# Kernel tuning notes

Measured on AMD Instinct MI355X. Metric: run time of the kernel, lower is better.

The kernel has to match this reference:

```python
import jax, jax.numpy as jnp
import numpy as np

S = 64            # rendered_size
CLASS_NUM = 14    # dataset.enc_len
NEG_SLOPE = 0.01
EPS = 1e-5


def _conv(x, w, stride, pad):
    return jax.lax.conv_general_dilated(
        x, w, (stride, stride), [(pad, pad), (pad, pad)],
        dimension_numbers=("NCHW", "OIHW", "NCHW"))


def _bn(x, gamma, beta):
    # BatchNorm2d in training mode: biased batch stats over (N,H,W)
    m = jnp.mean(x, axis=(0, 2, 3), keepdims=True)
    v = jnp.var(x, axis=(0, 2, 3), keepdims=True)
    xn = (x - m) * jax.lax.rsqrt(v + EPS)
    return xn * gamma.reshape(1, -1, 1, 1) + beta.reshape(1, -1, 1, 1)


def _lrelu(x):
    return jnp.where(x >= 0, x, NEG_SLOPE * x)


def _render(elements):
    # elements: (B, N, class_num+4)
    rects = elements[:, :, -4:]
    cls = elements[:, :, :-4]                       # (B, N, C)
    x = rects[:, :, 0][:, :, None, None] * S        # (B, N, 1, 1)
    y = rects[:, :, 1][:, :, None, None] * S
    w = rects[:, :, 2][:, :, None, None] * S
    h = rects[:, :, 3][:, :, None, None] * S
    x0, x1 = x - 0.5 * w, x + 0.5 * w
    y0, y1 = y - 0.5 * h, y + 0.5 * h
    cx = jnp.arange(S, dtype=elements.dtype)[None, None, None, :]  # varies along W
    cy = jnp.arange(S, dtype=elements.dtype)[None, None, :, None]  # varies along H
    k = lambda c, cr: jnp.maximum(1.0 - jnp.abs(c - cr), 0.0)
    b0 = lambda c, cr: jnp.clip(c - cr, 0.0, 1.0)
    b1 = lambda cr, c: jnp.clip(cr - c, 0.0, 1.0)
    by = b0(cy, y0) * b1(y1, cy)                    # (B, N, S, S)
    bx = b0(cx, x0) * b1(x1, cx)
    l0 = k(cx, x0) * by
    l1 = k(cx, x1) * by
    l2 = k(cy, y0) * bx
    l3 = k(cy, y1) * bx
    rendered = jnp.maximum(jnp.maximum(l0, l1), jnp.maximum(l2, l3))  # (B,N,S,S)
    # sum over elements of class one-hot * rendered -> (B, C, S, S)
    return jnp.einsum("bnc,bnhw->bchw", cls, rendered)


def setup_inputs() -> dict:
    key = jax.random.key(0)
    ks = jax.random.split(key, 8)
    B, N = 64, 46
    inp = {
        "input_data": jax.random.uniform(ks[0], (B, N, CLASS_NUM + 4), dtype=jnp.float32),
        "input_length": jax.random.randint(ks[1], (B,), 0, N, dtype=jnp.int32),
        # cnn convs (bias=False) + BN affine params
        "w1": jax.random.normal(ks[2], (64, CLASS_NUM, 5, 5), jnp.float32) * 0.05,
        "g1": jnp.ones((64,), jnp.float32), "b1": jnp.zeros((64,), jnp.float32),
        "w2": jax.random.normal(ks[3], (128, 64, 5, 5), jnp.float32) * 0.03,
        "g2": jnp.ones((128,), jnp.float32), "b2": jnp.zeros((128,), jnp.float32),
        "w3": jax.random.normal(ks[4], (256, 128, 5, 5), jnp.float32) * 0.02,
        "g3": jnp.ones((256,), jnp.float32), "b3": jnp.zeros((256,), jnp.float32),
        # classifier: conv k=8 (bias=False) + BN + 1x1 conv (bias=True)
        "w4": jax.random.normal(ks[5], (1024, 256, 8, 8), jnp.float32) * 0.01,
        "g4": jnp.ones((1024,), jnp.float32), "b4": jnp.zeros((1024,), jnp.float32),
        "w5": jax.random.normal(ks[6], (1, 1024, 1, 1), jnp.float32) * 0.03,
        "b5": jnp.zeros((1,), jnp.float32),
    }
    return inp


def reference(input_data, input_length, w1, g1, b1, w2, g2, b2,
              w3, g3, b3, w4, g4, b4, w5, b5):
    rendered = _render(input_data)                       # (B, C, 64, 64)
    h = _lrelu(_bn(_conv(rendered, w1, 2, 2), g1, b1))   # (B, 64, 32, 32)
    h = _lrelu(_bn(_conv(h, w2, 2, 2), g2, b2))          # (B, 128, 16, 16)
    h = _lrelu(_bn(_conv(h, w3, 2, 2), g3, b3))          # (B, 256, 8, 8)
    h = _lrelu(_bn(_conv(h, w4, 1, 0), g4, b4))          # (B, 1024, 1, 1)
    out = _conv(h, w5, 1, 0) + b5.reshape(1, -1, 1, 1)   # (B, 1, 1, 1)
    return out.squeeze()                                 # (B,)
```

## Files before the change

### kernel.cpp

```cpp
#include <hip/hip_runtime.h>
#include <hip/hip_bf16.h>

#define NEG 0.01f
#define EPS 1e-5f

typedef __attribute__((ext_vector_type(8))) short short8;
typedef __attribute__((ext_vector_type(4))) float floatx4;

__device__ inline unsigned short f2bf(float f) {
    __hip_bfloat16 h = __float2bfloat16(f);
    union { __hip_bfloat16 h; unsigned short u; } cv; cv.h = h;
    return cv.u;
}

__global__ __launch_bounds__(256) void render_kernel(const float* __restrict__ in,
                                                     unsigned short* __restrict__ out) {
    int b = blockIdx.x >> 4;
    int chunk = blockIdx.x & 15;
    __shared__ float r0[46], r1[46], r2[46], r3[46];
    __shared__ float cls_s[46 * 14];
    int tid = threadIdx.x;
    if (tid < 46) {
        const float* p = in + ((size_t)b * 46 + tid) * 18 + 14;
        float x = p[0] * 64.f, y = p[1] * 64.f, w = p[2] * 64.f, h = p[3] * 64.f;
        r0[tid] = x - 0.5f * w; r1[tid] = x + 0.5f * w;
        r2[tid] = y - 0.5f * h; r3[tid] = y + 0.5f * h;
    }
    for (int idx = tid; idx < 46 * 14; idx += 256) {
        int n = idx / 14, c = idx % 14;
        cls_s[idx] = in[((size_t)b * 46 + n) * 18 + c];
    }
    __syncthreads();
    if (tid < 33) {
        int j = chunk * 33 + tid;
        if (j < 528) {
            int y, x;
            if (j < 136) { y = j / 68; x = j - y * 68; }
            else if (j < 272) { int t = j - 136; int yy = t / 68; y = 66 + yy; x = t - yy * 68; }
            else { int t = j - 272; y = 2 + (t >> 2); int k = t & 3; x = (k < 2) ? k : 64 + k; }
            size_t zb = (((size_t)b * 68 + y) * 68 + x) * 16;
            short8 z;
#pragma unroll
            for (int i = 0; i < 8; ++i) z[i] = 0;
            *(short8*)(out + zb) = z;
            *(short8*)(out + zb + 8) = z;
        }
    }
    int pix = chunk * 256 + tid;
    float cx = (float)(pix & 63);
    float cy = (float)(pix >> 6);
    float acc[14];
#pragma unroll
    for (int c = 0; c < 14; ++c) acc[c] = 0.f;
    for (int n = 0; n < 46; ++n) {
        float x0 = r0[n], x1 = r1[n], y0 = r2[n], y1 = r3[n];
        float by = fminf(fmaxf(cy - y0, 0.f), 1.f) * fminf(fmaxf(y1 - cy, 0.f), 1.f);
        float bx = fminf(fmaxf(cx - x0, 0.f), 1.f) * fminf(fmaxf(x1 - cx, 0.f), 1.f);
        float kx0 = fmaxf(1.f - fabsf(cx - x0), 0.f);
        float kx1 = fmaxf(1.f - fabsf(cx - x1), 0.f);
        float ky0 = fmaxf(1.f - fabsf(cy - y0), 0.f);
        float ky1 = fmaxf(1.f - fabsf(cy - y1), 0.f);
        float r = fmaxf(fmaxf(kx0 * by, kx1 * by), fmaxf(ky0 * bx, ky1 * bx));
        if (r > 0.f) {
#pragma unroll
            for (int c = 0; c < 14; ++c) acc[c] = fmaf(cls_s[n * 14 + c], r, acc[c]);
        }
    }
    size_t obase = (((size_t)b * 68 + ((pix >> 6) + 2)) * 68 + ((pix & 63) + 2)) * 16;
    short8 v0, v1;
#pragma unroll
    for (int i = 0; i < 8; ++i) v0[i] = (short)f2bf(acc[i]);
#pragma unroll
    for (int i = 0; i < 6; ++i) v1[i] = (short)f2bf(acc[8 + i]);
    v1[6] = 0; v1[7] = 0;
    *(short8*)(out + obase) = v0;
    *(short8*)(out + obase + 8) = v1;
}

__global__ __launch_bounds__(256) void wtrans_all(const float* __restrict__ w1,
                                                  const float* __restrict__ w2,
                                                  const float* __restrict__ w3,
                                                  unsigned short* __restrict__ wT1,
                                                  unsigned short* __restrict__ wT2,
                                                  unsigned short* __restrict__ wT3) {
    int idx = blockIdx.x * 256 + threadIdx.x;
    const float* w; unsigned short* wT; int CIN, CPLOG, SUB, COLOG;
    if (idx < 30720) { w = w1; wT = wT1; CIN = 14; CPLOG = 4; SUB = 3; COLOG = 6; }
    else if (idx < 235520) { idx -= 30720; w = w2; wT = wT2; CIN = 64; CPLOG = 6; SUB = 10; COLOG = 7; }
    else if (idx < 1054720) { idx -= 235520; w = w3; wT = wT3; CIN = 128; CPLOG = 7; SUB = 20; COLOG = 8; }
    else return;
    int kk = idx & 31;
    int co = (idx >> 5) & ((1 << COLOG) - 1);
    int s = idx >> (5 + COLOG);
    int kh = s / SUB, sub = s - kh * SUB;
    int kidx = sub * 32 + kk;
    int kw = kidx >> CPLOG;
    int ci = kidx & ((1 << CPLOG) - 1);
    float v = (kw < 5 && ci < CIN) ? w[((size_t)(co * CIN + ci) * 5 + kh) * 5 + kw] : 0.f;
    wT[idx] = f2bf(v);
}

template <int CP, int COUT, int HP, int LOG_OHW, int LOG_OW, int SUB,
          int NCO, int NT, int CH, int NW>
__global__ __launch_bounds__(NW * 64) void conv_mfma(
        const unsigned short* __restrict__ inP,
        const unsigned short* __restrict__ wT,
        float* __restrict__ outX,
        float* __restrict__ stacc) {
    constexpr int NSTEP = 5 * SUB;
    constexpr int NCHUNK = NSTEP / CH;
    constexpr int COT = NT * 16;
    constexpr int NSTG = (CH * COT * 4) / (NW * 64);
    static_assert(NSTEP % CH == 0, "CH must divide NSTEP");
    static_assert((CH * COT * 4) % (NW * 64) == 0, "staging must tile evenly");
    __shared__ short Bs[2][CH][COT][32];
    __shared__ float sred[NW][2][COT];
    int tid = threadIdx.x;
    int wave = tid >> 6, lane = tid & 63, q = lane >> 4, l16 = lane & 15;
    int bm = blockIdx.x / NCO, bco = blockIdx.x % NCO;

    const short* aB[4];
#pragma unroll
    for (int f = 0; f < 4; ++f) {
        int m = bm * (NW * 64) + wave * 64 + f * 16 + l16;
        int b = m >> LOG_OHW;
        int ohw = m & ((1 << LOG_OHW) - 1);
        int oh = ohw >> LOG_OW, ow = ohw & ((1 << LOG_OW) - 1);
        aB[f] = (const short*)inP + ((size_t)((b * HP + 2 * oh) * HP + 2 * ow)) * CP + q * 8;
    }
    const short* bgbase = (const short*)wT + (size_t)bco * COT * 32;

    floatx4 acc[4][NT];
#pragma unroll
    for (int f = 0; f < 4; ++f)
#pragma unroll
        for (int nt = 0; nt < NT; ++nt) acc[f][nt] = (floatx4){0.f, 0.f, 0.f, 0.f};

    short8 nb[NSTG];
#pragma unroll
    for (int i = 0; i < NSTG; ++i) {
        int v = tid + i * NW * 64;
        int s = v / (COT * 4);
        int rem = v - s * (COT * 4);
        nb[i] = *(const short8*)(bgbase + ((size_t)s * COUT) * 32 + rem * 8);
    }
#pragma unroll
    for (int i = 0; i < NSTG; ++i) {
        int v = tid + i * NW * 64;
        int s = v / (COT * 4);
        int rem = v - s * (COT * 4);
        *(short8*)((short*)&Bs[0][s][0][0] + rem * 8) = nb[i];
    }
    __syncthreads();

    for (int chunk = 0; chunk < NCHUNK; ++chunk) {
        int cur = chunk & 1;
        if (chunk + 1 < NCHUNK) {
            int step0 = (chunk + 1) * CH;
#pragma unroll
            for (int i = 0; i < NSTG; ++i) {
                int v = tid + i * NW * 64;
                int s = v / (COT * 4);
                int rem = v - s * (COT * 4);
                nb[i] = *(const short8*)(bgbase + ((size_t)(step0 + s) * COUT) * 32 + rem * 8);
            }
        }
#pragma unroll
        for (int s = 0; s < CH; ++s) {
            int step = chunk * CH + s;
            int kh = step / SUB, sub = step - kh * SUB;
            short8 af[4];
#pragma unroll
            for (int f = 0; f < 4; ++f)
                af[f] = *(const short8*)(aB[f] + (size_t)(kh * HP) * CP + sub * 32);
#pragma unroll
            for (int nt = 0; nt < NT; ++nt) {
                short8 bf = *(const short8*)&Bs[cur][s][nt * 16 + l16][q * 8];
#pragma unroll
                for (int f = 0; f < 4; ++f)
                    acc[f][nt] = __builtin_amdgcn_mfma_f32_16x16x32_bf16(af[f], bf, acc[f][nt], 0, 0, 0);
            }
        }
        if (chunk + 1 < NCHUNK) {
#pragma unroll
            for (int i = 0; i < NSTG; ++i) {
                int v = tid + i * NW * 64;
                int s = v / (COT * 4);
                int rem = v - s * (COT * 4);
                *(short8*)((short*)&Bs[cur ^ 1][s][0][0] + rem * 8) = nb[i];
            }
            __syncthreads();
        }
    }
#pragma unroll
    for (int f = 0; f < 4; ++f)
#pragma unroll
        for (int nt = 0; nt < NT; ++nt)
#pragma unroll
            for (int rg = 0; rg < 4; ++rg) {
                int mg = bm * (NW * 64) + wave * 64 + f * 16 + q * 4 + rg;
                int co = bco * COT + nt * 16 + l16;
                outX[(size_t)mg * COUT + co] = acc[f][nt][rg];
            }
#pragma unroll
    for (int nt = 0; nt < NT; ++nt) {
        float s = 0.f, s2 = 0.f;
#pragma unroll
        for (int f = 0; f < 4; ++f)
#pragma unroll
            for (int rg = 0; rg < 4; ++rg) {
                float v = acc[f][nt][rg];
                s += v; s2 = fmaf(v, v, s2);
            }
        s += __shfl_xor(s, 16); s += __shfl_xor(s, 32);
        s2 += __shfl_xor(s2, 16); s2 += __shfl_xor(s2, 32);
        if (q == 0) {
            sred[wave][0][nt * 16 + l16] = s;
            sred[wave][1][nt * 16 + l16] = s2;
        }
    }
    __syncthreads();
    if (tid < COT) {
        float ts = 0.f, ts2 = 0.f;
#pragma unroll
        for (int w = 0; w < NW; ++w) { ts += sred[w][0][tid]; ts2 += sred[w][1][tid]; }
        atomicAdd(&stacc[bco * COT + tid], ts);
        atomicAdd(&stacc[COUT + bco * COT + tid], ts2);
    }
}

__global__ __launch_bounds__(256) void conv4_mfma(const unsigned short* __restrict__ A,
                                                  const float* __restrict__ w4,
                                                  float* __restrict__ h4) {
    constexpr int CH = 4, NCHUNK = 8;
    __shared__ short Bs[CH][64][40];
    int tid = threadIdx.x;
    int bco = blockIdx.x & 15;
    int ks = blockIdx.x >> 4;
    int wave = tid >> 6, lane = tid & 63, q = lane >> 4, l16 = lane & 15;
    const short* aBase = (const short*)A + (size_t)(wave * 16 + l16) * 16384 + ks * 1024 + q * 8;
    int r = tid >> 2, cc = tid & 3;
    const float* bg = w4 + (size_t)(bco * 64 + r) * 16384 + ks * 1024 + cc * 8;

    floatx4 acc[4];
#pragma unroll
    for (int nt = 0; nt < 4; ++nt) acc[nt] = (floatx4){0.f, 0.f, 0.f, 0.f};

    short8 nb[CH];
#pragma unroll
    for (int s = 0; s < CH; ++s) {
        float4 b0 = *(const float4*)(bg + s * 32);
        float4 b1 = *(const float4*)(bg + s * 32 + 4);
        nb[s][0] = (short)f2bf(b0.x); nb[s][1] = (short)f2bf(b0.y);
        nb[s][2] = (short)f2bf(b0.z); nb[s][3] = (short)f2bf(b0.w);
        nb[s][4] = (short)f2bf(b1.x); nb[s][5] = (short)f2bf(b1.y);
        nb[s][6] = (short)f2bf(b1.z); nb[s][7] = (short)f2bf(b1.w);
    }
#pragma unroll
    for (int s = 0; s < CH; ++s) *(short8*)&Bs[s][r][cc * 8] = nb[s];
    __syncthreads();

    for (int chunk = 0; chunk < NCHUNK; ++chunk) {
        bool has_next = (chunk + 1 < NCHUNK);
        if (has_next) {
#pragma unroll
            for (int s = 0; s < CH; ++s) {
                int step = (chunk + 1) * CH + s;
                float4 b0 = *(const float4*)(bg + step * 32);
                float4 b1 = *(const float4*)(bg + step * 32 + 4);
                nb[s][0] = (short)f2bf(b0.x); nb[s][1] = (short)f2bf(b0.y);
                nb[s][2] = (short)f2bf(b0.z); nb[s][3] = (short)f2bf(b0.w);
                nb[s][4] = (short)f2bf(b1.x); nb[s][5] = (short)f2bf(b1.y);
                nb[s][6] = (short)f2bf(b1.z); nb[s][7] = (short)f2bf(b1.w);
            }
        }
#pragma unroll
        for (int s = 0; s < CH; ++s) {
            int step = chunk * CH + s;
            short8 af = *(const short8*)(aBase + step * 32);
#pragma unroll
            for (int nt = 0; nt < 4; ++nt) {
                short8 bf = *(const short8*)&Bs[s][nt * 16 + l16][q * 8];
                acc[nt] = __builtin_amdgcn_mfma_f32_16x16x32_bf16(af, bf, acc[nt], 0, 0, 0);
            }
        }
        if (has_next) {
            __syncthreads();
#pragma unroll
            for (int s = 0; s < CH; ++s) *(short8*)&Bs[s][r][cc * 8] = nb[s];
            __syncthreads();
        }
    }
#pragma unroll
    for (int nt = 0; nt < 4; ++nt) {
#pragma unroll
        for (int rg = 0; rg < 4; ++rg) {
            int mg = wave * 16 + q * 4 + rg;
            int co = bco * 64 + nt * 16 + l16;
            atomicAdd(&h4[(size_t)mg * 1024 + co], acc[nt][rg]);
        }
    }
}

__global__ __launch_bounds__(256) void stats_part(const float* __restrict__ X,
                                                  float* __restrict__ acc,
                                                  int CO, int R, int RPB, int CGLOG) {
    int tid = threadIdx.x;
    int cg = blockIdx.x & ((1 << CGLOG) - 1);
    int rb = blockIdx.x >> CGLOG;
    int c = (cg << 6) + (tid & 63);
    int w = tid >> 6;
    float s = 0.f, s2 = 0.f;
    int rend = min(R, (rb + 1) * RPB);
    for (int r = rb * RPB + w; r < rend; r += 4) {
        float v = X[(size_t)r * CO + c];
        s += v; s2 += v * v;
    }
    __shared__ float ls[4][64], ls2[4][64];
    ls[w][tid & 63] = s; ls2[w][tid & 63] = s2;
    __syncthreads();
    if (tid < 64) {
        float ts = ls[0][tid] + ls[1][tid] + ls[2][tid] + ls[3][tid];
        float ts2 = ls2[0][tid] + ls2[1][tid] + ls2[2][tid] + ls2[3][tid];
        int cc = (cg << 6) + tid;
        atomicAdd(&acc[cc], ts);
        atomicAdd(&acc[CO + cc], ts2);
    }
}

__global__ __launch_bounds__(256) void bnpad_kernel(const float* __restrict__ X,
                                                    const float* __restrict__ stacc,
                                                    const float* __restrict__ g,
                                                    const float* __restrict__ bb,
                                                    unsigned short* __restrict__ out,
                                                    int CO_LOG, int OH, int OHP,
                                                    float invN, int total) {
    int idx = blockIdx.x * 256 + threadIdx.x;
    if (idx >= total) return;
    int CO = 1 << CO_LOG;
    int c = idx & (CO - 1);
    float mean = stacc[c] * invN;
    float var = fmaxf(stacc[CO + c] * invN - mean * mean, 0.f);
    float sc = g[c] * rsqrtf(var + EPS);
    float sh = bb[c] - mean * sc;
    int t = idx >> CO_LOG;
    int x = t % OHP; t /= OHP;
    int y = t % OHP; int b = t / OHP;
    unsigned short v = 0;
    if (y >= 2 && y < OH + 2 && x >= 2 && x < OH + 2) {
        float f = X[(((size_t)(b * OH + (y - 2)) * OH + (x - 2)) << CO_LOG) + c];
        f = f * sc + sh;
        f = f >= 0.f ? f : NEG * f;
        v = f2bf(f);
    }
    out[idx] = v;
}

__global__ __launch_bounds__(256) void bn_nchw_kernel(const float* __restrict__ X,
                                                      const float* __restrict__ stacc,
                                                      const float* __restrict__ g,
                                                      const float* __restrict__ bb,
                                                      unsigned short* __restrict__ out,
                                                      int total) {
    int idx = blockIdx.x * 256 + threadIdx.x;
    if (idx >= total) return;
    int hw = idx & 63;
    int ci = (idx >> 6) & 255;
    int b = idx >> 14;
    float mean = stacc[ci] * (1.f / 4096.f);
    float var = fmaxf(stacc[256 + ci] * (1.f / 4096.f) - mean * mean, 0.f);
    float sc = g[ci] * rsqrtf(var + EPS);
    float sh = bb[ci] - mean * sc;
    float f = X[((size_t)(b * 64 + hw)) * 256 + ci] * sc + sh;
    f = f >= 0.f ? f : NEG * f;
    out[idx] = f2bf(f);
}

__global__ __launch_bounds__(256) void conv5_kernel(const float* __restrict__ X,
                                                    const float* __restrict__ stacc,
                                                    const float* __restrict__ g,
                                                    const float* __restrict__ bb,
                                                    const float* __restrict__ w5,
                                                    const float* __restrict__ b5,
                                                    float* __restrict__ out) {
    int b = blockIdx.x, tid = threadIdx.x;
    float s = 0.f;
    for (int c = tid; c < 1024; c += 256) {
        float mean = stacc[c] * (1.f / 64.f);
        float var = fmaxf(stacc[1024 + c] * (1.f / 64.f) - mean * mean, 0.f);
        float sc = g[c] * rsqrtf(var + EPS);
        float sh = bb[c] - mean * sc;
        float f = X[(size_t)b * 1024 + c] * sc + sh;
        f = f >= 0.f ? f : NEG * f;
        s = fmaf(f, w5[c], s);
    }
#pragma unroll
    for (int off = 32; off > 0; off >>= 1) s += __shfl_down(s, off);
    __shared__ float ls[4];
    if ((tid & 63) == 0) ls[tid >> 6] = s;
    __syncthreads();
    if (tid == 0) out[b] = ls[0] + ls[1] + ls[2] + ls[3] + b5[0];
}

extern "C" void kernel_launch(void* const* d_in, const int* in_sizes, int n_in,
                              void* d_out, int out_size, void* d_ws, size_t ws_size,
                              hipStream_t stream) {
    (void)in_sizes; (void)n_in; (void)out_size; (void)ws_size;
    const float* input_data = (const float*)d_in[0];
    const float* w1 = (const float*)d_in[2];
    const float* g1 = (const float*)d_in[3];
    const float* b1 = (const float*)d_in[4];
    const float* w2 = (const float*)d_in[5];
    const float* g2 = (const float*)d_in[6];
    const float* b2 = (const float*)d_in[7];
    const float* w3 = (const float*)d_in[8];
    const float* g3 = (const float*)d_in[9];
    const float* b3 = (const float*)d_in[10];
    const float* w4 = (const float*)d_in[11];
    const float* g4 = (const float*)d_in[12];
    const float* b4 = (const float*)d_in[13];
    const float* w5 = (const float*)d_in[14];
    const float* b5 = (const float*)d_in[15];

    char* ws = (char*)d_ws;
    float* regA = (float*)ws;
    char* wsB = ws + 16777216;
    char* wsC = wsB + 10616832;
    char* wsD = wsC + 9469952;
    float* h4  = (float*)wsD;
    float* st1 = (float*)(wsD + 262144);
    float* st2 = (float*)(wsD + 262656);
    float* st3 = (float*)(wsD + 263680);
    float* st4 = (float*)(wsD + 265728);
    unsigned short* wT1 = (unsigned short*)(wsD + 274432);
    unsigned short* wT2 = (unsigned short*)(wsD + 335872);
    unsigned short* wT3 = (unsigned short*)(wsD + 745472);

    unsigned short* rendered = (unsigned short*)wsC;
    float* conv1out = regA;
    unsigned short* pad1 = (unsigned short*)wsB;
    float* conv2out = (float*)wsC;
    unsigned short* pad2 = (unsigned short*)wsB;
    float* conv3out = regA;
    unsigned short* a4 = (unsigned short*)wsC;

    hipMemsetAsync(wsD, 0, 273920, stream);
    wtrans_all<<<4120, 256, 0, stream>>>(w1, w2, w3, wT1, wT2, wT3);
    render_kernel<<<1024, 256, 0, stream>>>(input_data, rendered);

    conv_mfma<16, 64, 68, 10, 5, 3, 1, 4, 5, 4><<<256, 256, 0, stream>>>(rendered, wT1, conv1out, st1);
    bnpad_kernel<<<20736, 256, 0, stream>>>(conv1out, st1, g1, b1, pad1, 6, 32, 36, 1.f / 65536.f, 5308416);

    conv_mfma<64, 128, 36, 8, 4, 10, 4, 2, 10, 4><<<256, 256, 0, stream>>>(pad1, wT2, conv2out, st2);
    bnpad_kernel<<<12800, 256, 0, stream>>>(conv2out, st2, g2, b2, pad2, 7, 16, 20, 1.f / 16384.f, 3276800);

    conv_mfma<128, 256, 20, 6, 3, 20, 8, 2, 10, 2><<<256, 128, 0, stream>>>(pad2, wT3, conv3out, st3);
    bn_nchw_kernel<<<4096, 256, 0, stream>>>(conv3out, st3, g3, b3, a4, 1048576);

    conv4_mfma<<<256, 256, 0, stream>>>(a4, w4, h4);
    stats_part<<<16, 256, 0, stream>>>(h4, st4, 1024, 64, 64, 4);

    conv5_kernel<<<64, 256, 0, stream>>>(h4, st4, g4, b4, w5, b5, (float*)d_out);
}
```

Before: 278.9 us.

## Stream conv weight fragments directly from global memory instead of LDS staging

All conv kernels drop the double-buffered LDS staging of weight tiles and the __syncthreads barriers. Each lane now loads its B fragments straight from global memory every k-step, and the k loop is fully unrolled over kh and sub. Tile shapes change: conv2 and conv3 use fewer waves with wider output-channel tiles per wave, and conv4 becomes a single-wave kernel that computes 4x4 MFMA tiles per lane. This removes barrier and LDS traffic, but weights are re-read from global memory or L2 by more waves, grids keep only 256 blocks of 1 to 4 waves, and register pressure rises.

```diff
diff --git a/kernel.cpp b/kernel.cpp
--- a/kernel.cpp
+++ b/kernel.cpp
@@ -101,19 +101,13 @@
 }
 
 template <int CP, int COUT, int HP, int LOG_OHW, int LOG_OW, int SUB,
-          int NCO, int NT, int CH, int NW>
-__global__ __launch_bounds__(NW * 64) void conv_mfma(
+          int NCO, int NT, int NW>
+__global__ __launch_bounds__(NW * 64) void conv_stream(
         const unsigned short* __restrict__ inP,
         const unsigned short* __restrict__ wT,
         float* __restrict__ outX,
         float* __restrict__ stacc) {
-    constexpr int NSTEP = 5 * SUB;
-    constexpr int NCHUNK = NSTEP / CH;
     constexpr int COT = NT * 16;
-    constexpr int NSTG = (CH * COT * 4) / (NW * 64);
-    static_assert(NSTEP % CH == 0, "CH must divide NSTEP");
-    static_assert((CH * COT * 4) % (NW * 64) == 0, "staging must tile evenly");
-    __shared__ short Bs[2][CH][COT][32];
     __shared__ float sred[NW][2][COT];
     int tid = threadIdx.x;
     int wave = tid >> 6, lane = tid & 63, q = lane >> 4, l16 = lane & 15;
@@ -128,7 +122,7 @@
         int oh = ohw >> LOG_OW, ow = ohw & ((1 << LOG_OW) - 1);
         aB[f] = (const short*)inP + ((size_t)((b * HP + 2 * oh) * HP + 2 * ow)) * CP + q * 8;
     }
-    const short* bgbase = (const short*)wT + (size_t)bco * COT * 32;
+    const short* bB = (const short*)wT + (size_t)(bco * COT + l16) * 32 + q * 8;
 
     floatx4 acc[4][NT];
 #pragma unroll
@@ -136,60 +130,24 @@
 #pragma unroll
         for (int nt = 0; nt < NT; ++nt) acc[f][nt] = (floatx4){0.f, 0.f, 0.f, 0.f};
 
-    short8 nb[NSTG];
-#pragma unroll
-    for (int i = 0; i < NSTG; ++i) {
-        int v = tid + i * NW * 64;
-        int s = v / (COT * 4);
-        int rem = v - s * (COT * 4);
-        nb[i] = *(const short8*)(bgbase + ((size_t)s * COUT) * 32 + rem * 8);
-    }
-#pragma unroll
-    for (int i = 0; i < NSTG; ++i) {
-        int v = tid + i * NW * 64;
-        int s = v / (COT * 4);
-        int rem = v - s * (COT * 4);
-        *(short8*)((short*)&Bs[0][s][0][0] + rem * 8) = nb[i];
-    }
-    __syncthreads();
-
-    for (int chunk = 0; chunk < NCHUNK; ++chunk) {
-        int cur = chunk & 1;
-        if (chunk + 1 < NCHUNK) {
-            int step0 = (chunk + 1) * CH;
-#pragma unroll
-            for (int i = 0; i < NSTG; ++i) {
-                int v = tid + i * NW * 64;
-                int s = v / (COT * 4);
-                int rem = v - s * (COT * 4);
-                nb[i] = *(const short8*)(bgbase + ((size_t)(step0 + s) * COUT) * 32 + rem * 8);
-            }
-        }
-#pragma unroll
-        for (int s = 0; s < CH; ++s) {
-            int step = chunk * CH + s;
-            int kh = step / SUB, sub = step - kh * SUB;
+#pragma unroll
+    for (int kh = 0; kh < 5; ++kh) {
+#pragma unroll
+        for (int sub = 0; sub < SUB; ++sub) {
+            int step = kh * SUB + sub;
             short8 af[4];
 #pragma unroll
             for (int f = 0; f < 4; ++f)
                 af[f] = *(const short8*)(aB[f] + (size_t)(kh * HP) * CP + sub * 32);
-#pragma unroll
-            for (int nt = 0; nt < NT; ++nt) {
-                short8 bf = *(const short8*)&Bs[cur][s][nt * 16 + l16][q * 8];
+            short8 bf[NT];
+#pragma unroll
+            for (int nt = 0; nt < NT; ++nt)
+                bf[nt] = *(const short8*)(bB + (size_t)step * COUT * 32 + nt * 512);
+#pragma unroll
+            for (int nt = 0; nt < NT; ++nt)
 #pragma unroll
                 for (int f = 0; f < 4; ++f)
-                    acc[f][nt] = __builtin_amdgcn_mfma_f32_16x16x32_bf16(af[f], bf, acc[f][nt], 0, 0, 0);
-            }
-        }
-        if (chunk + 1 < NCHUNK) {
-#pragma unroll
-            for (int i = 0; i < NSTG; ++i) {
-                int v = tid + i * NW * 64;
-                int s = v / (COT * 4);
-                int rem = v - s * (COT * 4);
-                *(short8*)((short*)&Bs[cur ^ 1][s][0][0] + rem * 8) = nb[i];
-            }
-            __syncthreads();
+                    acc[f][nt] = __builtin_amdgcn_mfma_f32_16x16x32_bf16(af[f], bf[nt], acc[f][nt], 0, 0, 0);
         }
     }
 #pragma unroll
@@ -202,6 +160,7 @@
                 int co = bco * COT + nt * 16 + l16;
                 outX[(size_t)mg * COUT + co] = acc[f][nt][rg];
             }
+    float ps[NT], ps2[NT];
 #pragma unroll
     for (int nt = 0; nt < NT; ++nt) {
         float s = 0.f, s2 = 0.f;
@@ -214,92 +173,87 @@
             }
         s += __shfl_xor(s, 16); s += __shfl_xor(s, 32);
         s2 += __shfl_xor(s2, 16); s2 += __shfl_xor(s2, 32);
+        ps[nt] = s; ps2[nt] = s2;
+    }
+    if (NW == 1) {
         if (q == 0) {
-            sred[wave][0][nt * 16 + l16] = s;
-            sred[wave][1][nt * 16 + l16] = s2;
-        }
-    }
-    __syncthreads();
-    if (tid < COT) {
-        float ts = 0.f, ts2 = 0.f;
-#pragma unroll
-        for (int w = 0; w < NW; ++w) { ts += sred[w][0][tid]; ts2 += sred[w][1][tid]; }
-        atomicAdd(&stacc[bco * COT + tid], ts);
-        atomicAdd(&stacc[COUT + bco * COT + tid], ts2);
-    }
-}
-
-__global__ __launch_bounds__(256) void conv4_mfma(const unsigned short* __restrict__ A,
-                                                  const float* __restrict__ w4,
-                                                  float* __restrict__ h4) {
-    constexpr int CH = 4, NCHUNK = 8;
-    __shared__ short Bs[CH][64][40];
-    int tid = threadIdx.x;
+#pragma unroll
+            for (int nt = 0; nt < NT; ++nt) {
+                int co = bco * COT + nt * 16 + l16;
+                atomicAdd(&stacc[co], ps[nt]);
+                atomicAdd(&stacc[COUT + co], ps2[nt]);
+            }
+        }
+    } else {
+        if (q == 0) {
+#pragma unroll
+            for (int nt = 0; nt < NT; ++nt) {
+                sred[wave][0][nt * 16 + l16] = ps[nt];
+                sred[wave][1][nt * 16 + l16] = ps2[nt];
+            }
+        }
+        __syncthreads();
+        if (tid < COT) {
+            float ts = 0.f, ts2 = 0.f;
+#pragma unroll
+            for (int w = 0; w < NW; ++w) { ts += sred[w][0][tid]; ts2 += sred[w][1][tid]; }
+            atomicAdd(&stacc[bco * COT + tid], ts);
+            atomicAdd(&stacc[COUT + bco * COT + tid], ts2);
+        }
+    }
+}
+
+__global__ __launch_bounds__(64) void conv4_stream(const unsigned short* __restrict__ A,
+                                                   const float* __restrict__ w4,
+                                                   float* __restrict__ h4) {
+    int lane = threadIdx.x, q = lane >> 4, l16 = lane & 15;
     int bco = blockIdx.x & 15;
     int ks = blockIdx.x >> 4;
-    int wave = tid >> 6, lane = tid & 63, q = lane >> 4, l16 = lane & 15;
-    const short* aBase = (const short*)A + (size_t)(wave * 16 + l16) * 16384 + ks * 1024 + q * 8;
-    int r = tid >> 2, cc = tid & 3;
-    const float* bg = w4 + (size_t)(bco * 64 + r) * 16384 + ks * 1024 + cc * 8;
-
-    floatx4 acc[4];
-#pragma unroll
-    for (int nt = 0; nt < 4; ++nt) acc[nt] = (floatx4){0.f, 0.f, 0.f, 0.f};
-
-    short8 nb[CH];
-#pragma unroll
-    for (int s = 0; s < CH; ++s) {
-        float4 b0 = *(const float4*)(bg + s * 32);
-        float4 b1 = *(const float4*)(bg + s * 32 + 4);
-        nb[s][0] = (short)f2bf(b0.x); nb[s][1] = (short)f2bf(b0.y);
-        nb[s][2] = (short)f2bf(b0.z); nb[s][3] = (short)f2bf(b0.w);
-        nb[s][4] = (short)f2bf(b1.x); nb[s][5] = (short)f2bf(b1.y);
-        nb[s][6] = (short)f2bf(b1.z); nb[s][7] = (short)f2bf(b1.w);
-    }
-#pragma unroll
-    for (int s = 0; s < CH; ++s) *(short8*)&Bs[s][r][cc * 8] = nb[s];
-    __syncthreads();
-
-    for (int chunk = 0; chunk < NCHUNK; ++chunk) {
-        bool has_next = (chunk + 1 < NCHUNK);
-        if (has_next) {
-#pragma unroll
-            for (int s = 0; s < CH; ++s) {
-                int step = (chunk + 1) * CH + s;
-                float4 b0 = *(const float4*)(bg + step * 32);
-                float4 b1 = *(const float4*)(bg + step * 32 + 4);
-                nb[s][0] = (short)f2bf(b0.x); nb[s][1] = (short)f2bf(b0.y);
-                nb[s][2] = (short)f2bf(b0.z); nb[s][3] = (short)f2bf(b0.w);
-                nb[s][4] = (short)f2bf(b1.x); nb[s][5] = (short)f2bf(b1.y);
-                nb[s][6] = (short)f2bf(b1.z); nb[s][7] = (short)f2bf(b1.w);
+    const short* aB[4];
+#pragma unroll
+    for (int f = 0; f < 4; ++f)
+        aB[f] = (const short*)A + (size_t)(f * 16 + l16) * 16384 + ks * 1024 + q * 8;
+    const float* bB = w4 + (size_t)(bco * 64 + l16) * 16384 + ks * 1024 + q * 8;
+
+    floatx4 acc[4][4];
+#pragma unroll
+    for (int f = 0; f < 4; ++f)
+#pragma unroll
+        for (int nt = 0; nt < 4; ++nt) acc[f][nt] = (floatx4){0.f, 0.f, 0.f, 0.f};
+
+#pragma unroll 8
+    for (int step = 0; step < 32; ++step) {
+        short8 af[4];
+#pragma unroll
+        for (int f = 0; f < 4; ++f)
+            af[f] = *(const short8*)(aB[f] + step * 32);
+        short8 bf[4];
+#pragma unroll
+        for (int nt = 0; nt < 4; ++nt) {
+            const float* p = bB + (size_t)nt * 16 * 16384 + step * 32;
+            float4 b0 = *(const float4*)p;
+            float4 b1 = *(const float4*)(p + 4);
+            bf[nt][0] = (short)f2bf(b0.x); bf[nt][1] = (short)f2bf(b0.y);
+            bf[nt][2] = (short)f2bf(b0.z); bf[nt][3] = (short)f2bf(b0.w);
+            bf[nt][4] = (short)f2bf(b1.x); bf[nt][5] = (short)f2bf(b1.y);
+            bf[nt][6] = (short)f2bf(b1.z); bf[nt][7] = (short)f2bf(b1.w);
+        }
+#pragma unroll
+        for (int nt = 0; nt < 4; ++nt)
+#pragma unroll
+            for (int f = 0; f < 4; ++f)
+                acc[f][nt] = __builtin_amdgcn_mfma_f32_16x16x32_bf16(af[f], bf[nt], acc[f][nt], 0, 0, 0);
+    }
+#pragma unroll
+    for (int f = 0; f < 4; ++f)
+#pragma unroll
+        for (int nt = 0; nt < 4; ++nt)
+#pragma unroll
+            for (int rg = 0; rg < 4; ++rg) {
+                int mg = f * 16 + q * 4 + rg;
+                int co = bco * 64 + nt * 16 + l16;
+                atomicAdd(&h4[(size_t)mg * 1024 + co], acc[f][nt][rg]);
             }
-        }
-#pragma unroll
-        for (int s = 0; s < CH; ++s) {
-            int step = chunk * CH + s;
-            short8 af = *(const short8*)(aBase + step * 32);
-#pragma unroll
-            for (int nt = 0; nt < 4; ++nt) {
-                short8 bf = *(const short8*)&Bs[s][nt * 16 + l16][q * 8];
-                acc[nt] = __builtin_amdgcn_mfma_f32_16x16x32_bf16(af, bf, acc[nt], 0, 0, 0);
-            }
-        }
-        if (has_next) {
-            __syncthreads();
-#pragma unroll
-            for (int s = 0; s < CH; ++s) *(short8*)&Bs[s][r][cc * 8] = nb[s];
-            __syncthreads();
-        }
-    }
-#pragma unroll
-    for (int nt = 0; nt < 4; ++nt) {
-#pragma unroll
-        for (int rg = 0; rg < 4; ++rg) {
-            int mg = wave * 16 + q * 4 + rg;
-            int co = bco * 64 + nt * 16 + l16;
-            atomicAdd(&h4[(size_t)mg * 1024 + co], acc[nt][rg]);
-        }
-    }
 }
 
 __global__ __launch_bounds__(256) void stats_part(const float* __restrict__ X,
@@ -448,16 +402,16 @@
     wtrans_all<<<4120, 256, 0, stream>>>(w1, w2, w3, wT1, wT2, wT3);
     render_kernel<<<1024, 256, 0, stream>>>(input_data, rendered);
 
-    conv_mfma<16, 64, 68, 10, 5, 3, 1, 4, 5, 4><<<256, 256, 0, stream>>>(rendered, wT1, conv1out, st1);
+    conv_stream<16, 64, 68, 10, 5, 3, 1, 4, 4><<<256, 256, 0, stream>>>(rendered, wT1, conv1out, st1);
     bnpad_kernel<<<20736, 256, 0, stream>>>(conv1out, st1, g1, b1, pad1, 6, 32, 36, 1.f / 65536.f, 5308416);
 
-    conv_mfma<64, 128, 36, 8, 4, 10, 4, 2, 10, 4><<<256, 256, 0, stream>>>(pad1, wT2, conv2out, st2);
+    conv_stream<64, 128, 36, 8, 4, 10, 2, 4, 2><<<256, 128, 0, stream>>>(pad1, wT2, conv2out, st2);
     bnpad_kernel<<<12800, 256, 0, stream>>>(conv2out, st2, g2, b2, pad2, 7, 16, 20, 1.f / 16384.f, 3276800);
 
-    conv_mfma<128, 256, 20, 6, 3, 20, 8, 2, 10, 2><<<256, 128, 0, stream>>>(pad2, wT3, conv3out, st3);
+    conv_stream<128, 256, 20, 6, 3, 20, 4, 4, 1><<<256, 64, 0, stream>>>(pad2, wT3, conv3out, st3);
     bn_nchw_kernel<<<4096, 256, 0, stream>>>(conv3out, st3, g3, b3, a4, 1048576);
 
-    conv4_mfma<<<256, 256, 0, stream>>>(a4, w4, h4);
+    conv4_stream<<<256, 64, 0, stream>>>(a4, w4, h4);
     stats_part<<<16, 256, 0, stream>>>(h4, st4, 1024, 64, 64, 4);
 
     conv5_kernel<<<64, 256, 0, stream>>>(h4, st4, g4, b4, w5, b5, (float*)d_out);
```

Result: slower. 365.4 us (+31.0%).

## Split-K conv2 and conv3 into partial buffers to raise block parallelism

Applied to the files above, without the earlier changes.

Adds a conv_split kernel that divides the reduction steps of conv2 (2-way) and conv3 (4-way) across extra blocks, launching 1024 blocks of 128 threads instead of 256 blocks. Each split writes its partial outputs to its own buffer. Separate stats_part launches then sum the partials and compute BN statistics, and the BN/pad kernels also sum the partials. This is meant to fill more compute units on the mid-size convolutions, at the cost of extra partial-output traffic, re-reading the partials twice, and two extra kernel launches. The workspace layout is rearranged so the partial buffers do not alias each other.

```diff
diff --git a/kernel.cpp b/kernel.cpp
--- a/kernel.cpp
+++ b/kernel.cpp
@@ -111,8 +111,6 @@
     constexpr int NCHUNK = NSTEP / CH;
     constexpr int COT = NT * 16;
     constexpr int NSTG = (CH * COT * 4) / (NW * 64);
-    static_assert(NSTEP % CH == 0, "CH must divide NSTEP");
-    static_assert((CH * COT * 4) % (NW * 64) == 0, "staging must tile evenly");
     __shared__ short Bs[2][CH][COT][32];
     __shared__ float sred[NW][2][COT];
     int tid = threadIdx.x;
@@ -227,6 +225,114 @@
         atomicAdd(&stacc[bco * COT + tid], ts);
         atomicAdd(&stacc[COUT + bco * COT + tid], ts2);
     }
+}
+
+template <int CP, int COUT, int HP, int LOG_OHW, int LOG_OW, int SUB,
+          int NM, int NCO, int NT, int CH, int NW, int KS>
+__global__ __launch_bounds__(NW * 64) void conv_split(
+        const unsigned short* __restrict__ inP,
+        const unsigned short* __restrict__ wT,
+        float* __restrict__ outP) {
+    constexpr int NSTEP = 5 * SUB;
+    constexpr int SSTEP = NSTEP / KS;
+    constexpr int NCHUNK = SSTEP / CH;
+    constexpr int COT = NT * 16;
+    constexpr int NSTG = (CH * COT * 4) / (NW * 64);
+    constexpr int M = NM * NW * 64;
+    static_assert(NSTEP % KS == 0 && SSTEP % CH == 0, "split tiling");
+    __shared__ short Bs[2][CH][COT][32];
+    int tid = threadIdx.x;
+    int wave = tid >> 6, lane = tid & 63, q = lane >> 4, l16 = lane & 15;
+    int bidx = blockIdx.x;
+    int ks = bidx / (NM * NCO);
+    int rem = bidx - ks * (NM * NCO);
+    int bm = rem / NCO, bco = rem % NCO;
+    int sbase = ks * SSTEP;
+
+    const short* aB[4];
+#pragma unroll
+    for (int f = 0; f < 4; ++f) {
+        int m = bm * (NW * 64) + wave * 64 + f * 16 + l16;
+        int b = m >> LOG_OHW;
+        int ohw = m & ((1 << LOG_OHW) - 1);
+        int oh = ohw >> LOG_OW, ow = ohw & ((1 << LOG_OW) - 1);
+        aB[f] = (const short*)inP + ((size_t)((b * HP + 2 * oh) * HP + 2 * ow)) * CP + q * 8;
+    }
+    const short* bgbase = (const short*)wT + (size_t)bco * COT * 32;
+
+    floatx4 acc[4][NT];
+#pragma unroll
+    for (int f = 0; f < 4; ++f)
+#pragma unroll
+        for (int nt = 0; nt < NT; ++nt) acc[f][nt] = (floatx4){0.f, 0.f, 0.f, 0.f};
+
+    short8 nb[NSTG];
+#pragma unroll
+    for (int i = 0; i < NSTG; ++i) {
+        int v = tid + i * NW * 64;
+        int s = v / (COT * 4);
+        int rem2 = v - s * (COT * 4);
+        nb[i] = *(const short8*)(bgbase + ((size_t)(sbase + s) * COUT) * 32 + rem2 * 8);
+    }
+#pragma unroll
+    for (int i = 0; i < NSTG; ++i) {
+        int v = tid + i * NW * 64;
+        int s = v / (COT * 4);
+        int rem2 = v - s * (COT * 4);
+        *(short8*)((short*)&Bs[0][s][0][0] + rem2 * 8) = nb[i];
+    }
+    __syncthreads();
+
+    for (int chunk = 0; chunk < NCHUNK; ++chunk) {
+        int cur = chunk & 1;
+        if (chunk + 1 < NCHUNK) {
+            int step0 = sbase + (chunk + 1) * CH;
+#pragma unroll
+            for (int i = 0; i < NSTG; ++i) {
+                int v = tid + i * NW * 64;
+                int s = v / (COT * 4);
+                int rem2 = v - s * (COT * 4);
+                nb[i] = *(const short8*)(bgbase + ((size_t)(step0 + s) * COUT) * 32 + rem2 * 8);
+            }
+        }
+#pragma unroll
+        for (int s = 0; s < CH; ++s) {
+            int gstep = sbase + chunk * CH + s;
+            int kh = gstep / SUB, sub = gstep - kh * SUB;
+            short8 af[4];
+#pragma unroll
+            for (int f = 0; f < 4; ++f)
+                af[f] = *(const short8*)(aB[f] + (size_t)(kh * HP) * CP + sub * 32);
+#pragma unroll
+            for (int nt = 0; nt < NT; ++nt) {
+                short8 bf = *(const short8*)&Bs[cur][s][nt * 16 + l16][q * 8];
+#pragma unroll
+                for (int f = 0; f < 4; ++f)
+                    acc[f][nt] = __builtin_amdgcn_mfma_f32_16x16x32_bf16(af[f], bf, acc[f][nt], 0, 0, 0);
+            }
+        }
+        if (chunk + 1 < NCHUNK) {
+#pragma unroll
+            for (int i = 0; i < NSTG; ++i) {
+                int v = tid + i * NW * 64;
+                int s = v / (COT * 4);
+                int rem2 = v - s * (COT * 4);
+                *(short8*)((short*)&Bs[cur ^ 1][s][0][0] + rem2 * 8) = nb[i];
+            }
+            __syncthreads();
+        }
+    }
+    float* outK = outP + (size_t)ks * M * COUT;
+#pragma unroll
+    for (int f = 0; f < 4; ++f)
+#pragma unroll
+        for (int nt = 0; nt < NT; ++nt)
+#pragma unroll
+            for (int rg = 0; rg < 4; ++rg) {
+                int mg = bm * (NW * 64) + wave * 64 + f * 16 + q * 4 + rg;
+                int co = bco * COT + nt * 16 + l16;
+                outK[(size_t)mg * COUT + co] = acc[f][nt][rg];
+            }
 }
 
 __global__ __launch_bounds__(256) void conv4_mfma(const unsigned short* __restrict__ A,
@@ -304,7 +410,8 @@
 
 __global__ __launch_bounds__(256) void stats_part(const float* __restrict__ X,
                                                   float* __restrict__ acc,
-                                                  int CO, int R, int RPB, int CGLOG) {
+                                                  int CO, int R, int RPB, int CGLOG,
+                                                  int nsplit, size_t kstride) {
     int tid = threadIdx.x;
     int cg = blockIdx.x & ((1 << CGLOG) - 1);
     int rb = blockIdx.x >> CGLOG;
@@ -313,7 +420,8 @@
     float s = 0.f, s2 = 0.f;
     int rend = min(R, (rb + 1) * RPB);
     for (int r = rb * RPB + w; r < rend; r += 4) {
-        float v = X[(size_t)r * CO + c];
+        float v = 0.f;
+        for (int t = 0; t < nsplit; ++t) v += X[(size_t)t * kstride + (size_t)r * CO + c];
         s += v; s2 += v * v;
     }
     __shared__ float ls[4][64], ls2[4][64];
@@ -334,7 +442,8 @@
                                                     const float* __restrict__ bb,
                                                     unsigned short* __restrict__ out,
                                                     int CO_LOG, int OH, int OHP,
-                                                    float invN, int total) {
+                                                    float invN, int total,
+                                                    int nsplit, size_t kstride) {
     int idx = blockIdx.x * 256 + threadIdx.x;
     if (idx >= total) return;
     int CO = 1 << CO_LOG;
@@ -348,7 +457,9 @@
     int y = t % OHP; int b = t / OHP;
     unsigned short v = 0;
     if (y >= 2 && y < OH + 2 && x >= 2 && x < OH + 2) {
-        float f = X[(((size_t)(b * OH + (y - 2)) * OH + (x - 2)) << CO_LOG) + c];
+        size_t base = (((size_t)(b * OH + (y - 2)) * OH + (x - 2)) << CO_LOG) + c;
+        float f = 0.f;
+        for (int ts = 0; ts < nsplit; ++ts) f += X[base + (size_t)ts * kstride];
         f = f * sc + sh;
         f = f >= 0.f ? f : NEG * f;
         v = f2bf(f);
@@ -361,7 +472,7 @@
                                                       const float* __restrict__ g,
                                                       const float* __restrict__ bb,
                                                       unsigned short* __restrict__ out,
-                                                      int total) {
+                                                      int total, int nsplit, size_t kstride) {
     int idx = blockIdx.x * 256 + threadIdx.x;
     if (idx >= total) return;
     int hw = idx & 63;
@@ -371,7 +482,10 @@
     float var = fmaxf(stacc[256 + ci] * (1.f / 4096.f) - mean * mean, 0.f);
     float sc = g[ci] * rsqrtf(var + EPS);
     float sh = bb[ci] - mean * sc;
-    float f = X[((size_t)(b * 64 + hw)) * 256 + ci] * sc + sh;
+    size_t base = ((size_t)(b * 64 + hw)) * 256 + ci;
+    float f = 0.f;
+    for (int ts = 0; ts < nsplit; ++ts) f += X[base + (size_t)ts * kstride];
+    f = f * sc + sh;
     f = f >= 0.f ? f : NEG * f;
     out[idx] = f2bf(f);
 }
@@ -423,42 +537,41 @@
     const float* b5 = (const float*)d_in[15];
 
     char* ws = (char*)d_ws;
-    float* regA = (float*)ws;
-    char* wsB = ws + 16777216;
-    char* wsC = wsB + 10616832;
-    char* wsD = wsC + 9469952;
-    float* h4  = (float*)wsD;
-    float* st1 = (float*)(wsD + 262144);
-    float* st2 = (float*)(wsD + 262656);
-    float* st3 = (float*)(wsD + 263680);
-    float* st4 = (float*)(wsD + 265728);
-    unsigned short* wT1 = (unsigned short*)(wsD + 274432);
-    unsigned short* wT2 = (unsigned short*)(wsD + 335872);
-    unsigned short* wT3 = (unsigned short*)(wsD + 745472);
-
-    unsigned short* rendered = (unsigned short*)wsC;
-    float* conv1out = regA;
-    unsigned short* pad1 = (unsigned short*)wsB;
-    float* conv2out = (float*)wsC;
-    unsigned short* pad2 = (unsigned short*)wsB;
-    float* conv3out = regA;
-    unsigned short* a4 = (unsigned short*)wsC;
-
-    hipMemsetAsync(wsD, 0, 273920, stream);
+    unsigned short* rendered   = (unsigned short*)(ws + 0);
+    float*          conv1out   = (float*)(ws + 9469952);
+    unsigned short* pad1       = (unsigned short*)(ws + 26247168);
+    float*          conv2parts = (float*)(ws + 36864000);
+    unsigned short* pad2       = (unsigned short*)(ws + 53641216);
+    float*          conv3parts = (float*)(ws + 60194816);
+    unsigned short* a4         = (unsigned short*)(ws + 76972032);
+    float*          h4         = (float*)(ws + 79069184);
+    float*          st1        = (float*)(ws + 79331328);
+    float*          st2        = (float*)(ws + 79331840);
+    float*          st3        = (float*)(ws + 79332864);
+    float*          st4        = (float*)(ws + 79334912);
+    unsigned short* wT1        = (unsigned short*)(ws + 79343104);
+    unsigned short* wT2        = (unsigned short*)(ws + 79404544);
+    unsigned short* wT3        = (unsigned short*)(ws + 79814144);
+
+    hipMemsetAsync(ws + 79069184, 0, 273920, stream);
     wtrans_all<<<4120, 256, 0, stream>>>(w1, w2, w3, wT1, wT2, wT3);
     render_kernel<<<1024, 256, 0, stream>>>(input_data, rendered);
 
     conv_mfma<16, 64, 68, 10, 5, 3, 1, 4, 5, 4><<<256, 256, 0, stream>>>(rendered, wT1, conv1out, st1);
-    bnpad_kernel<<<20736, 256, 0, stream>>>(conv1out, st1, g1, b1, pad1, 6, 32, 36, 1.f / 65536.f, 5308416);
-
-    conv_mfma<64, 128, 36, 8, 4, 10, 4, 2, 10, 4><<<256, 256, 0, stream>>>(pad1, wT2, conv2out, st2);
-    bnpad_kernel<<<12800, 256, 0, stream>>>(conv2out, st2, g2, b2, pad2, 7, 16, 20, 1.f / 16384.f, 3276800);
-
-    conv_mfma<128, 256, 20, 6, 3, 20, 8, 2, 10, 2><<<256, 128, 0, stream>>>(pad2, wT3, conv3out, st3);
-    bn_nchw_kernel<<<4096, 256, 0, stream>>>(conv3out, st3, g3, b3, a4, 1048576);
+    bnpad_kernel<<<20736, 256, 0, stream>>>(conv1out, st1, g1, b1, pad1, 6, 32, 36,
+                                            1.f / 65536.f, 5308416, 1, 0);
+
+    conv_split<64, 128, 36, 8, 4, 10, 128, 4, 2, 5, 2, 2><<<1024, 128, 0, stream>>>(pad1, wT2, conv2parts);
+    stats_part<<<256, 256, 0, stream>>>(conv2parts, st2, 128, 16384, 128, 1, 2, 2097152);
+    bnpad_kernel<<<12800, 256, 0, stream>>>(conv2parts, st2, g2, b2, pad2, 7, 16, 20,
+                                            1.f / 16384.f, 3276800, 2, 2097152);
+
+    conv_split<128, 256, 20, 6, 3, 20, 32, 8, 2, 5, 2, 4><<<1024, 128, 0, stream>>>(pad2, wT3, conv3parts);
+    stats_part<<<512, 256, 0, stream>>>(conv3parts, st3, 256, 4096, 32, 2, 4, 1048576);
+    bn_nchw_kernel<<<4096, 256, 0, stream>>>(conv3parts, st3, g3, b3, a4, 1048576, 4, 1048576);
 
     conv4_mfma<<<256, 256, 0, stream>>>(a4, w4, h4);
-    stats_part<<<16, 256, 0, stream>>>(h4, st4, 1024, 64, 64, 4);
+    stats_part<<<16, 256, 0, stream>>>(h4, st4, 1024, 64, 64, 4, 1, 0);
 
     conv5_kernel<<<64, 256, 0, stream>>>(h4, st4, g4, b4, w5, b5, (float*)d_out);
 }
```

New measurement: 318.6 us. 14.2% more time.
